# Kernel tuning notes

Hardware: AMD Instinct MI355X
Metric: run time of the kernel (lower is better)

## Reference

```python
import jax, jax.numpy as jnp
import numpy as np

B, N, S, K = 8, 4096, 1024, 16
C_IN, C_OUT = 128, 256
BN_EPS = 1e-5


def setup_inputs() -> dict:
    key = jax.random.key(0)
    ks = jax.random.split(key, 20)
    sc = 0.02
    p = {
        'xyz': jax.random.normal(ks[0], (B, N, 3), jnp.float32),
        'points': jax.random.normal(ks[1], (B, N, C_IN), jnp.float32),
        'wq': jax.random.normal(ks[2], (C_IN, C_OUT), jnp.float32) * sc,
        'wk': jax.random.normal(ks[3], (C_IN, C_OUT), jnp.float32) * sc,
        'wv': jax.random.normal(ks[4], (C_IN, C_OUT), jnp.float32) * sc,
        'dw1': jax.random.normal(ks[5], (3, C_OUT), jnp.float32) * sc,
        'db1': jnp.zeros((C_OUT,), jnp.float32),
        'dw2': jax.random.normal(ks[6], (C_OUT, C_OUT), jnp.float32) * sc,
        'db2': jnp.zeros((C_OUT,), jnp.float32),
        'gw1': jax.random.normal(ks[7], (C_OUT, C_OUT), jnp.float32) * sc,
        'gb1': jnp.zeros((C_OUT,), jnp.float32),
        'gw2': jax.random.normal(ks[8], (C_OUT, C_OUT), jnp.float32) * sc,
        'gb2': jnp.zeros((C_OUT,), jnp.float32),
        'lw': jax.random.normal(ks[9], (C_OUT, C_OUT), jnp.float32) * sc,
        'lb': jnp.zeros((C_OUT,), jnp.float32),
        'bn_g': jnp.ones((C_OUT,), jnp.float32),
        'bn_b': jnp.zeros((C_OUT,), jnp.float32),
    }
    return p


def _fps(xyz, npoint):
    # xyz: [N,3] -> farthest point sample indices [npoint] (deterministic start at 0,
    # matching torch impl with fixed seed semantics)
    n = xyz.shape[0]
    def step(carry, _):
        dist, far = carry
        centroid = xyz[far]                      # [3]
        d = jnp.sum((xyz - centroid) ** 2, -1)   # [N]
        dist = jnp.minimum(dist, d)
        return (dist, jnp.argmax(dist).astype(jnp.int32)), far
    init = (jnp.full((n,), 1e10, xyz.dtype), jnp.int32(0))
    _, idx = jax.lax.scan(step, init, None, length=npoint)
    return idx  # [npoint]


def _mlp2(x, w1, b1, w2, b2):
    return jax.nn.relu(x @ w1 + b1) @ w2 + b2


def reference(xyz, points, wq, wk, wv, dw1, db1, dw2, db2,
              gw1, gb1, gw2, gb2, lw, lb, bn_g, bn_b):
    # --- sample_and_group (FPS + KNN, knn=True) ---
    fps_idx = jax.vmap(lambda x: _fps(x, S))(xyz)                 # [B,S]
    new_xyz = jnp.take_along_axis(xyz, fps_idx[..., None], 1)     # [B,S,3]
    # squared distances sampled->all: [B,S,N]
    d2 = (jnp.sum(new_xyz**2, -1)[:, :, None]
          - 2.0 * jnp.einsum('bsc,bnc->bsn', new_xyz, xyz)
          + jnp.sum(xyz**2, -1)[:, None, :])
    knn_idx = jax.lax.top_k(-d2, K)[1]                            # [B,S,K]
    gather = jax.vmap(lambda a, i: a[i])
    knn_xyz = gather(xyz, knn_idx)                                # [B,S,K,3]
    knn_xyz_norm = knn_xyz - new_xyz[:, :, None]                  # centered coords
    knn_points = gather(points, knn_idx)                          # [B,S,K,C_in]
    sampled_points = jnp.take_along_axis(points, fps_idx[..., None], 1)  # [B,S,C_in]

    # --- vector attention ---
    q = sampled_points @ wq                                       # [B,S,C_out]
    k = knn_points @ wk                                           # [B,S,K,C_out]
    v = knn_points @ wv                                           # [B,S,K,C_out]
    pos_enc = _mlp2(knn_xyz_norm, dw1, db1, dw2, db2)             # [B,S,K,C_out]
    att = _mlp2(q[:, :, None] - k + pos_enc, gw1, gb1, gw2, gb2)  # [B,S,K,C_out]
    att = jax.nn.softmax(att / np.sqrt(C_OUT).astype(np.float32), axis=-2)
    res = jnp.einsum('bmnf,bmnf->bmf', att, v + pos_enc)          # [B,S,C_out]

    # --- fc_last + BatchNorm1d (training-mode batch stats, biased var) + ReLU ---
    res = res @ lw + lb
    mean = jnp.mean(res, axis=(0, 1))
    var = jnp.var(res, axis=(0, 1))
    res = bn_g * (res - mean) * jax.lax.rsqrt(var + BN_EPS) + bn_b
    res = jax.nn.relu(res)
    return new_xyz, res
```

## Files before the change

kernel.cpp:

```cpp
#include <hip/hip_runtime.h>

typedef unsigned long long ull;
typedef __attribute__((ext_vector_type(8))) short bf16x8;
typedef __attribute__((ext_vector_type(4))) float f32x4;

__device__ __forceinline__ unsigned short bf16b(float x){
    unsigned u = __float_as_uint(x);
    unsigned r = (u + 0x7FFFu + ((u >> 16) & 1u)) >> 16;
    return (unsigned short)r;
}
__device__ __forceinline__ float b2f(unsigned short u){
    return __uint_as_float(((unsigned)u) << 16);
}
__device__ __forceinline__ void st4(unsigned short* p, f32x4 v){
    ull pk = (ull)bf16b(v[0]) | (((ull)bf16b(v[1])) << 16)
           | (((ull)bf16b(v[2])) << 32) | (((ull)bf16b(v[3])) << 48);
    *(ull*)p = pk;
}
__device__ __forceinline__ f32x4 ld4(const unsigned short* p){
    ull pk = *(const ull*)p;
    f32x4 v;
    v[0] = b2f((unsigned short)pk);
    v[1] = b2f((unsigned short)(pk >> 16));
    v[2] = b2f((unsigned short)(pk >> 32));
    v[3] = b2f((unsigned short)(pk >> 48));
    return v;
}

#define DPPMAX(k, ctrl) do { \
    unsigned _lo = (unsigned)(k), _hi = (unsigned)((k) >> 32); \
    unsigned _l2 = (unsigned)__builtin_amdgcn_update_dpp((int)_lo, (int)_lo, (ctrl), 0xF, 0xF, false); \
    unsigned _h2 = (unsigned)__builtin_amdgcn_update_dpp((int)_hi, (int)_hi, (ctrl), 0xF, 0xF, false); \
    ull _k2 = (((ull)_h2) << 32) | _l2; \
    if (_k2 > (k)) (k) = _k2; \
} while (0)
#define DPPMIN(k, ctrl) do { \
    unsigned _lo = (unsigned)(k), _hi = (unsigned)((k) >> 32); \
    unsigned _l2 = (unsigned)__builtin_amdgcn_update_dpp((int)_lo, (int)_lo, (ctrl), 0xF, 0xF, false); \
    unsigned _h2 = (unsigned)__builtin_amdgcn_update_dpp((int)_hi, (int)_hi, (ctrl), 0xF, 0xF, false); \
    ull _k2 = (((ull)_h2) << 32) | _l2; \
    if (_k2 < (k)) (k) = _k2; \
} while (0)

template<int KT>
__device__ __forceinline__ int swz(int r, int c){
    return r * (KT * 32) + ((((c >> 3) + r) & (KT * 4 - 1)) << 3) + (c & 7);
}

template<int KT>
__device__ __forceinline__ void gemmT(const unsigned short* __restrict__ Wt,
                                      const unsigned short* __restrict__ Blds,
                                      int ch0, int lane, f32x4 acc[4][4])
{
    int i = lane & 15, q = lane >> 4;
#pragma unroll
    for (int kt = 0; kt < KT; kt++){
        int k0 = kt * 32 + q * 8;
        bf16x8 bfr[4], afr[4];
#pragma unroll
        for (int nt = 0; nt < 4; nt++)
            bfr[nt] = *(const bf16x8*)(Blds + swz<KT>(nt * 16 + i, k0));
#pragma unroll
        for (int mt = 0; mt < 4; mt++)
            afr[mt] = *(const bf16x8*)(Wt + (size_t)(ch0 + mt * 16 + i) * (KT * 32) + k0);
#pragma unroll
        for (int mt = 0; mt < 4; mt++)
#pragma unroll
            for (int nt = 0; nt < 4; nt++)
                acc[mt][nt] = __builtin_amdgcn_mfma_f32_16x16x32_bf16(afr[mt], bfr[nt], acc[mt][nt], 0, 0, 0);
    }
}

#define ZERO44(A) do { _Pragma("unroll") for (int _m = 0; _m < 4; _m++) \
    { _Pragma("unroll") for (int _n = 0; _n < 4; _n++) { A[_m][_n][0]=0.f;A[_m][_n][1]=0.f;A[_m][_n][2]=0.f;A[_m][_n][3]=0.f; } } } while(0)

#define CTRL_B(b)  ((b) << 4)
#define CTRL_AUX   (8 << 4)

__device__ __forceinline__ int ctrl_ld(const int* ctrl, int idx){
    return __hip_atomic_load(ctrl + idx, __ATOMIC_RELAXED, __HIP_MEMORY_SCOPE_AGENT);
}

__device__ __forceinline__ void knn_one(int t2, int G,
        const float* __restrict__ xyz, const float* __restrict__ nxyz,
        int* __restrict__ knn_idx, float* d2s, ull* kslot)
{
    int b = G >> 10;
    int lane = t2 & 63, wvi = t2 >> 6;
    float qx = nxyz[(size_t)G * 3], qy = nxyz[(size_t)G * 3 + 1], qz = nxyz[(size_t)G * 3 + 2];
    float qq = qx * qx + qy * qy + qz * qz;
    for (int j = 0; j < 16; j++){
        int p = t2 + (j << 8);
        const float* s = xyz + ((size_t)b * 4096 + p) * 3;
        float x = s[0], y = s[1], z = s[2];
        d2s[p] = qq - 2.f * (qx * x + qy * y + qz * z) + (x * x + y * y + z * z);
    }
    __syncthreads();
    for (int r = 0; r < 16; r++){
        ull best = ~0ull;
#pragma unroll
        for (int j = 0; j < 16; j++){
            int p = t2 + (j << 8);
            unsigned bb = __float_as_uint(d2s[p]);
            bb = (bb & 0x80000000u) ? ~bb : (bb | 0x80000000u);
            ull key = (((ull)bb) << 32) | (unsigned)p;
            if (key < best) best = key;
        }
        DPPMIN(best, 0xB1); DPPMIN(best, 0x4E); DPPMIN(best, 0x141);
        DPPMIN(best, 0x140); DPPMIN(best, 0x142); DPPMIN(best, 0x143);
        if (lane == 63) kslot[wvi] = best;
        __syncthreads();
        if (t2 == 0){
            ull bk = kslot[0];
            for (int w = 1; w < 4; w++) if (kslot[w] < bk) bk = kslot[w];
            int p = (int)(unsigned)bk;
            knn_idx[(size_t)G * 16 + r] = p;
            d2s[p] = 3.0e38f;
        }
        __syncthreads();
    }
}

__device__ void attn_unit(int t, char* base, int G0,
    const unsigned short* __restrict__ pts16,
    const float* __restrict__ xyz, const float* __restrict__ nxyz,
    const int* __restrict__ knn_idx, const float* __restrict__ qbuf,
    const unsigned short* __restrict__ wkT, const unsigned short* __restrict__ wvT,
    const unsigned short* __restrict__ dw2T, const unsigned short* __restrict__ gw1T,
    const unsigned short* __restrict__ gw2T,
    const float* __restrict__ dw1, const float* __restrict__ db1,
    const float* __restrict__ db2, const float* __restrict__ gb1, const float* __restrict__ gb2,
    unsigned short* __restrict__ resY)
{
    unsigned short* bufA = (unsigned short*)base;
    unsigned short* bufU = (unsigned short*)(base + 32768);
    int lane = t & 63, wave = t >> 6;
    int i = lane & 15, q = lane >> 4;
    int ch0 = wave * 64;
    unsigned short* ptsA = bufU;
    float* dw1s  = (float*)(bufU + 8192);
    float* db1s  = (float*)(bufU + 9728);
    float* xyznS = (float*)(bufU + 10240);
    int*   idxs  = (int*)  (bufU + 10624);

    if (t < 64) idxs[t] = knn_idx[G0 * 16 + t];
    dw1s[t] = dw1[t]; dw1s[256 + t] = dw1[256 + t]; dw1s[512 + t] = dw1[512 + t];
    db1s[t] = db1[t];
    __syncthreads();

    if (t < 64){
        int G = G0 + (t >> 4); int bb = G >> 10; int p = idxs[t];
        const float* xp = xyz + ((size_t)bb * 4096 + p) * 3;
        const float* nz = nxyz + (size_t)G * 3;
        xyznS[t * 3 + 0] = xp[0] - nz[0];
        xyznS[t * 3 + 1] = xp[1] - nz[1];
        xyznS[t * 3 + 2] = xp[2] - nz[2];
    }
    {
        int r = t >> 2, seg = t & 3;
        int G = G0 + (r >> 4); int bb = G >> 10; int p = idxs[r];
        const uint4* src = (const uint4*)(pts16 + ((size_t)bb * 4096 + p) * 128 + seg * 32);
#pragma unroll
        for (int j = 0; j < 4; j++){
            uint4 v = src[j];
            *(uint4*)(ptsA + swz<4>(r, seg * 32 + j * 8)) = v;
        }
    }
    __syncthreads();

    {
        int r = lane;
        int o0 = wave * 64;
        float x = xyznS[r * 3], y = xyznS[r * 3 + 1], z = xyznS[r * 3 + 2];
#pragma unroll
        for (int j = 0; j < 64; j += 4){
            int o = o0 + j;
            f32x4 v;
#pragma unroll
            for (int e = 0; e < 4; e++)
                v[e] = fmaxf(db1s[o + e] + x * dw1s[o + e] + y * dw1s[256 + o + e] + z * dw1s[512 + o + e], 0.f);
            st4(bufA + swz<8>(r, o), v);
        }
    }
    __syncthreads();

    f32x4 accP[4][4]; ZERO44(accP);
    gemmT<8>(dw2T, bufA, ch0, lane, accP);
#pragma unroll
    for (int mt = 0; mt < 4; mt++){
        f32x4 d2v = *(const f32x4*)(db2 + ch0 + mt * 16 + q * 4);
#pragma unroll
        for (int nt = 0; nt < 4; nt++) accP[mt][nt] += d2v;
    }
    f32x4 accK[4][4]; ZERO44(accK);
    gemmT<4>(wkT, ptsA, ch0, lane, accK);
    __syncthreads();

#pragma unroll
    for (int mt = 0; mt < 4; mt++){
        int c = ch0 + mt * 16 + q * 4;
#pragma unroll
        for (int nt = 0; nt < 4; nt++){
            int r = nt * 16 + i;
            f32x4 qv = *(const f32x4*)(qbuf + (size_t)(G0 + nt) * 256 + c);
            f32x4 tv = qv - accK[mt][nt] + accP[mt][nt];
            st4(bufA + swz<8>(r, c), tv);
        }
    }
    f32x4 accV[4][4]; ZERO44(accV);
    gemmT<4>(wvT, ptsA, ch0, lane, accV);
    __syncthreads();

#pragma unroll
    for (int mt = 0; mt < 4; mt++){
        int c = ch0 + mt * 16 + q * 4;
#pragma unroll
        for (int nt = 0; nt < 4; nt++){
            int r = nt * 16 + i;
            f32x4 uv = accV[mt][nt] + accP[mt][nt];
            st4(bufU + swz<8>(r, c), uv);
        }
    }
    f32x4 acc1[4][4]; ZERO44(acc1);
    gemmT<8>(gw1T, bufA, ch0, lane, acc1);
    __syncthreads();

#pragma unroll
    for (int mt = 0; mt < 4; mt++){
        int c = ch0 + mt * 16 + q * 4;
        f32x4 g1v = *(const f32x4*)(gb1 + c);
#pragma unroll
        for (int nt = 0; nt < 4; nt++){
            int r = nt * 16 + i;
            f32x4 av = acc1[mt][nt] + g1v;
#pragma unroll
            for (int e = 0; e < 4; e++) av[e] = fmaxf(av[e], 0.f);
            st4(bufA + swz<8>(r, c), av);
        }
    }
    __syncthreads();

    f32x4 acc2[4][4]; ZERO44(acc2);
    gemmT<8>(gw2T, bufA, ch0, lane, acc2);
    __syncthreads();

#pragma unroll
    for (int mt = 0; mt < 4; mt++){
        int c = ch0 + mt * 16 + q * 4;
        f32x4 g2v = *(const f32x4*)(gb2 + c);
#pragma unroll
        for (int nt = 0; nt < 4; nt++){
            int r = nt * 16 + i;
            f32x4 ev;
#pragma unroll
            for (int e = 0; e < 4; e++) ev[e] = __expf((acc2[mt][nt][e] + g2v[e]) * 0.0625f);
            st4(bufA + swz<8>(r, c), ev);
        }
    }
    __syncthreads();

    {
        int g = t >> 6, c4 = (t & 63) * 4;
        f32x4 num; num[0]=0.f;num[1]=0.f;num[2]=0.f;num[3]=0.f;
        f32x4 den = num;
#pragma unroll
        for (int rr = 0; rr < 16; rr++){
            int r = g * 16 + rr;
            f32x4 e4 = ld4(bufA + swz<8>(r, c4));
            f32x4 u4 = ld4(bufU + swz<8>(r, c4));
            num += e4 * u4;
            den += e4;
        }
        f32x4 rv = num / den;
        st4(resY + (size_t)(G0 + g) * 256 + c4, rv);
    }
}

__device__ void do_chunk(int t, int c, char* SM,
    const float* __restrict__ xyz, const float* __restrict__ nxyz,
    const float* __restrict__ points, const float* __restrict__ wqT,
    const int* __restrict__ fps_idx, int* __restrict__ knn_idx, float* __restrict__ qbuf,
    const unsigned short* __restrict__ pts16,
    const unsigned short* __restrict__ wkT, const unsigned short* __restrict__ wvT,
    const unsigned short* __restrict__ dw2T, const unsigned short* __restrict__ gw1T,
    const unsigned short* __restrict__ gw2T,
    const float* __restrict__ dw1, const float* __restrict__ db1,
    const float* __restrict__ db2, const float* __restrict__ gb1, const float* __restrict__ gb2,
    unsigned short* __restrict__ resY)
{
    int g0 = c * 8;
    int sub = t >> 8, t2 = t & 255;
    float* d2s = (float*)(SM + sub * 16384);
    ull* kslot = (ull*)(SM + 131072) + sub * 4;
    for (int r4 = 0; r4 < 4; r4++)
        knn_one(t2, g0 + r4 * 2 + sub, xyz, nxyz, knn_idx, d2s, kslot);
    __syncthreads();
    {
        float* sp = (float*)SM;
        if (t < 256){
            int r = t >> 5, c4 = (t & 31) * 4;
            int G = g0 + r; int b = G >> 10; int p = fps_idx[G];
            *(f32x4*)(sp + r * 128 + c4) = *(const f32x4*)(points + ((size_t)b * 4096 + p) * 128 + c4);
        }
        __syncthreads();
        float acc[4] = {0.f, 0.f, 0.f, 0.f};
        const float* wr = wqT + t2 * 128;
        for (int k = 0; k < 128; k += 4){
            f32x4 w = *(const f32x4*)(wr + k);
#pragma unroll
            for (int r = 0; r < 4; r++){
                const float* row = sp + (sub * 4 + r) * 128;
                acc[r] += w[0]*row[k] + w[1]*row[k+1] + w[2]*row[k+2] + w[3]*row[k+3];
            }
        }
#pragma unroll
        for (int r = 0; r < 4; r++) qbuf[(size_t)(g0 + sub * 4 + r) * 256 + t2] = acc[r];
        __syncthreads();
    }
    attn_unit(t2, SM + sub * 65536, g0 + sub * 4, pts16, xyz, nxyz, knn_idx, qbuf,
              wkT, wvT, dw2T, gw1T, gw2T, dw1, db1, db2, gb1, gb2, resY);
    __syncthreads();
}

__global__ void init_ctrl(int* __restrict__ ctrl)
{
    ctrl[threadIdx.x] = 0;
}

__global__ __launch_bounds__(512, 2) void mega(
    const float* __restrict__ xyz, float* __restrict__ nxyz_out, int* __restrict__ fps_idx,
    const float* __restrict__ pts, unsigned short* __restrict__ pts16,
    const float* __restrict__ wq, const float* __restrict__ wk, const float* __restrict__ wv,
    const float* __restrict__ dw2, const float* __restrict__ gw1, const float* __restrict__ gw2,
    const float* __restrict__ lw,
    float* __restrict__ wqT, unsigned short* __restrict__ wkT, unsigned short* __restrict__ wvT,
    unsigned short* __restrict__ dw2T, unsigned short* __restrict__ gw1T,
    unsigned short* __restrict__ gw2T, unsigned short* __restrict__ lwT,
    float* __restrict__ stats,
    const float* __restrict__ dw1, const float* __restrict__ db1, const float* __restrict__ db2,
    const float* __restrict__ gb1, const float* __restrict__ gb2,
    int* __restrict__ knn_idx, float* __restrict__ qbuf, unsigned short* __restrict__ resY,
    int* __restrict__ ctrl)
{
    __shared__ __align__(16) char SM[132096];
    int blk = blockIdx.x, t = threadIdx.x;

    if (blk < 8){
        int b = blk;
        int lane = t & 63, wvi = t >> 6;
        float* sx = (float*)SM;
        float* sy = (float*)(SM + 16384);
        float* sz = (float*)(SM + 32768);
        int* farS = (int*)(SM + 49152);
        ull (*slotK)[8] = (ull(*)[8])(SM + 53248);
        for (int p = t; p < 4096; p += 512){
            const float* s = xyz + ((size_t)b * 4096 + p) * 3;
            sx[p] = s[0]; sy[p] = s[1]; sz[p] = s[2];
        }
        __syncthreads();
        float px[8], py[8], pz[8], dist[8];
        unsigned nplo[8];
#pragma unroll
        for (int j = 0; j < 8; j++){
            int p = t + (j << 9);
            px[j] = sx[p]; py[j] = sy[p]; pz[j] = sz[p];
            dist[j] = 1e10f;
            nplo[j] = ~(unsigned)p;
            asm volatile("" : "+v"(px[j]), "+v"(py[j]), "+v"(pz[j]), "+v"(nplo[j]));
        }
        int far = 0;
        float cx = sx[0], cy = sy[0], cz = sz[0];
        int par = 0;
        for (int s = 0; s < 1024; s++){
            if (t == 0) farS[s] = far;
            ull lb = 0;
#pragma unroll
            for (int j = 0; j < 8; j++){
                float dx = __fsub_rn(px[j], cx);
                float dy = __fsub_rn(py[j], cy);
                float dz = __fsub_rn(pz[j], cz);
                float d = __fadd_rn(__fadd_rn(__fmul_rn(dx, dx), __fmul_rn(dy, dy)), __fmul_rn(dz, dz));
                float nd = fminf(dist[j], d);
                dist[j] = nd;
                ull k2 = (((ull)__float_as_uint(nd)) << 32) | nplo[j];
                if (k2 > lb) lb = k2;
            }
            DPPMAX(lb, 0xB1); DPPMAX(lb, 0x4E); DPPMAX(lb, 0x141);
            DPPMAX(lb, 0x140); DPPMAX(lb, 0x142); DPPMAX(lb, 0x143);
            if (lane == 63) slotK[par][wvi] = lb;
            __syncthreads();
            ull k = slotK[par][lane & 7];
            DPPMAX(k, 0xB1); DPPMAX(k, 0x4E); DPPMAX(k, 0x141);
            far = (int)(~(unsigned)k);
            cx = sx[far]; cy = sy[far]; cz = sz[far];
            if (((s & 15) == 15) && wvi == 7){
                int s0 = s - 15;
                if (lane < 16){
                    fps_idx[b * 1024 + s0 + lane] = farS[s0 + lane];
                } else {
                    int idx = lane - 16;
                    int st = s0 + idx / 3, d = idx - (idx / 3) * 3;
                    int f = farS[st];
                    float v = (d == 0) ? sx[f] : ((d == 1) ? sy[f] : sz[f]);
                    nxyz_out[(size_t)b * 3072 + st * 3 + d] = v;
                }
                if (lane == 0)
                    __hip_atomic_store(ctrl + CTRL_B(b), s + 1,
                                       __ATOMIC_RELEASE, __HIP_MEMORY_SCOPE_AGENT);
            }
            par ^= 1;
        }
        if (t == 0){ while (ctrl_ld(ctrl, CTRL_AUX) < 248) __builtin_amdgcn_s_sleep(16); }
        __syncthreads();
        __threadfence();
        do_chunk(t, b * 128 + 127, SM, xyz, nxyz_out, pts, wqT, fps_idx, knn_idx, qbuf,
                 pts16, wkT, wvT, dw2T, gw1T, gw2T, dw1, db1, db2, gb1, gb2, resY);
        return;
    }

    int w = blk - 8;
    for (int base = w; base < 704; base += 248){
        if (base == 0) stats[t & 511] = 0.f;
        int i = base * 512 + t;
        if (i < 32768){ int n = i >> 7, kk = i & 127; wqT[i] = wq[kk * 256 + n]; }
        else if (i < 65536){ int j = i - 32768; int n = j >> 7, kk = j & 127; wkT[j] = bf16b(wk[kk * 256 + n]); }
        else if (i < 98304){ int j = i - 65536; int n = j >> 7, kk = j & 127; wvT[j] = bf16b(wv[kk * 256 + n]); }
        else if (i < 163840){ int j = i - 98304; int n = j >> 8, kk = j & 255; dw2T[j] = bf16b(dw2[kk * 256 + n]); }
        else if (i < 229376){ int j = i - 163840; int n = j >> 8, kk = j & 255; gw1T[j] = bf16b(gw1[kk * 256 + n]); }
        else if (i < 294912){ int j = i - 229376; int n = j >> 8, kk = j & 255; gw2T[j] = bf16b(gw2[kk * 256 + n]); }
        else { int j = i - 294912; int n = j >> 8, kk = j & 255; lwT[j] = bf16b(lw[kk * 256 + n]); }
    }
    for (int base = w; base < 2048; base += 248){
        int i = (base * 512 + t) * 4;
        f32x4 v = *(const f32x4*)(pts + i);
        ull pk = (ull)bf16b(v[0]) | (((ull)bf16b(v[1])) << 16)
               | (((ull)bf16b(v[2])) << 32) | (((ull)bf16b(v[3])) << 48);
        *(ull*)(pts16 + i) = pk;
    }
    __threadfence();
    __syncthreads();
    if (t == 0){
        atomicAdd(ctrl + CTRL_AUX, 1);
        while (ctrl_ld(ctrl, CTRL_AUX) < 248) __builtin_amdgcn_s_sleep(16);
    }
    __syncthreads();
    __threadfence();
    for (int j = 0; j < 5; j++){
        int p = w + 248 * j;
        if (p >= 1016) break;
        int bb = p & 7, cc = p >> 3;
        int need = cc * 8 + 8;
        if (t == 0){ while (ctrl_ld(ctrl, CTRL_B(bb)) < need) __builtin_amdgcn_s_sleep(8); }
        __syncthreads();
        __threadfence();
        do_chunk(t, bb * 128 + cc, SM, xyz, nxyz_out, pts, wqT, fps_idx, knn_idx, qbuf,
                 pts16, wkT, wvT, dw2T, gw1T, gw2T, dw1, db1, db2, gb1, gb2, resY);
    }
}

__global__ __launch_bounds__(256, 2) void z_gemm(const unsigned short* __restrict__ resY,
                                                 const unsigned short* __restrict__ lwT,
                                                 const float* __restrict__ lb,
                                                 float* __restrict__ zbuf,
                                                 float* __restrict__ stats)
{
    int t = threadIdx.x, lane = t & 63, wave = t >> 6;
    int i = lane & 15, q = lane >> 4;
    int row0 = blockIdx.x * 128;
    int ch0 = wave * 64;
    f32x4 acc[4][8];
#pragma unroll
    for (int mt = 0; mt < 4; mt++)
#pragma unroll
        for (int nt = 0; nt < 8; nt++){ acc[mt][nt][0]=0.f;acc[mt][nt][1]=0.f;acc[mt][nt][2]=0.f;acc[mt][nt][3]=0.f; }
#pragma unroll
    for (int kt = 0; kt < 8; kt++){
        int k0 = kt * 32 + q * 8;
        bf16x8 a[4], bb[8];
#pragma unroll
        for (int mt = 0; mt < 4; mt++)
            a[mt] = *(const bf16x8*)(lwT + (size_t)(ch0 + mt * 16 + i) * 256 + k0);
#pragma unroll
        for (int nt = 0; nt < 8; nt++)
            bb[nt] = *(const bf16x8*)(resY + (size_t)(row0 + nt * 16 + i) * 256 + k0);
#pragma unroll
        for (int mt = 0; mt < 4; mt++)
#pragma unroll
            for (int nt = 0; nt < 8; nt++)
                acc[mt][nt] = __builtin_amdgcn_mfma_f32_16x16x32_bf16(a[mt], bb[nt], acc[mt][nt], 0, 0, 0);
    }
    f32x4 s1[4], s2[4];
#pragma unroll
    for (int mt = 0; mt < 4; mt++){ s1[mt][0]=0.f;s1[mt][1]=0.f;s1[mt][2]=0.f;s1[mt][3]=0.f; s2[mt]=s1[mt]; }
#pragma unroll
    for (int mt = 0; mt < 4; mt++){
        int c = ch0 + mt * 16 + q * 4;
        f32x4 lb4 = *(const f32x4*)(lb + c);
#pragma unroll
        for (int nt = 0; nt < 8; nt++){
            int r = row0 + nt * 16 + i;
            f32x4 z = acc[mt][nt] + lb4;
            *(f32x4*)(zbuf + (size_t)r * 256 + c) = z;
            s1[mt] += z;
            s2[mt] += z * z;
        }
    }
    for (int m = 1; m < 16; m <<= 1){
#pragma unroll
        for (int mt = 0; mt < 4; mt++)
#pragma unroll
            for (int e = 0; e < 4; e++){
                s1[mt][e] += __shfl_xor(s1[mt][e], m);
                s2[mt][e] += __shfl_xor(s2[mt][e], m);
            }
    }
    if (i == 0){
#pragma unroll
        for (int mt = 0; mt < 4; mt++){
            int c = ch0 + mt * 16 + q * 4;
#pragma unroll
            for (int e = 0; e < 4; e++){
                atomicAdd(&stats[c + e], s1[mt][e]);
                atomicAdd(&stats[256 + c + e], s2[mt][e]);
            }
        }
    }
}

__global__ __launch_bounds__(256) void bn_kernel(const float* __restrict__ zbuf,
                                                 const float* __restrict__ stats,
                                                 const float* __restrict__ bn_g,
                                                 const float* __restrict__ bn_b,
                                                 float* __restrict__ out)
{
    int G = blockIdx.x, c = threadIdx.x;
    float mean = stats[c] * (1.f / 8192.f);
    float var = stats[256 + c] * (1.f / 8192.f) - mean * mean;
    float inv = rsqrtf(var + 1e-5f);
    float z = zbuf[(size_t)G * 256 + c];
    float y = bn_g[c] * (z - mean) * inv + bn_b[c];
    out[24576 + (size_t)G * 256 + c] = fmaxf(y, 0.f);
}

extern "C" void kernel_launch(void* const* d_in, const int* in_sizes, int n_in,
                              void* d_out, int out_size, void* d_ws, size_t ws_size,
                              hipStream_t stream)
{
    const float* xyz    = (const float*)d_in[0];
    const float* points = (const float*)d_in[1];
    const float* wq  = (const float*)d_in[2];
    const float* wk  = (const float*)d_in[3];
    const float* wv  = (const float*)d_in[4];
    const float* dw1 = (const float*)d_in[5];
    const float* db1 = (const float*)d_in[6];
    const float* dw2 = (const float*)d_in[7];
    const float* db2 = (const float*)d_in[8];
    const float* gw1 = (const float*)d_in[9];
    const float* gb1 = (const float*)d_in[10];
    const float* gw2 = (const float*)d_in[11];
    const float* gb2 = (const float*)d_in[12];
    const float* lw  = (const float*)d_in[13];
    const float* lb  = (const float*)d_in[14];
    const float* bn_g = (const float*)d_in[15];
    const float* bn_b = (const float*)d_in[16];
    float* out = (float*)d_out;

    char* ws = (char*)d_ws;
    int*            fps_idx = (int*)(ws + 0);
    int*            knn_idx = (int*)(ws + 32768);
    float*          qbuf    = (float*)(ws + 557056);
    unsigned short* pts16   = (unsigned short*)(ws + 8945664);
    unsigned short* wkT     = (unsigned short*)(ws + 17334272);
    unsigned short* wvT     = (unsigned short*)(ws + 17399808);
    unsigned short* dw2T    = (unsigned short*)(ws + 17465344);
    unsigned short* gw1T    = (unsigned short*)(ws + 17596416);
    unsigned short* gw2T    = (unsigned short*)(ws + 17727488);
    unsigned short* lwT     = (unsigned short*)(ws + 17858560);
    float*          wqT     = (float*)(ws + 17989632);
    unsigned short* resY    = (unsigned short*)(ws + 18120704);
    float*          zbuf    = (float*)(ws + 22315008);
    float*          stats   = (float*)(ws + 30703616);
    int*            ctrl    = (int*)(ws + 22315008);

    init_ctrl<<<1, 256, 0, stream>>>(ctrl);
    mega<<<256, 512, 0, stream>>>(xyz, out, fps_idx, points, pts16,
                                  wq, wk, wv, dw2, gw1, gw2, lw,
                                  wqT, wkT, wvT, dw2T, gw1T, gw2T, lwT, stats,
                                  dw1, db1, db2, gb1, gb2,
                                  knn_idx, qbuf, resY, ctrl);
    z_gemm<<<64, 256, 0, stream>>>(resY, lwT, lb, zbuf, stats);
    bn_kernel<<<8192, 256, 0, stream>>>(zbuf, stats, bn_g, bn_b, out);
}
```

Before: 989.9 us.

## Replace per-batch FPS progress counter with sentinel-polled data readiness

Consumer blocks used to wait on a per-batch release counter before each chunk. Now fps_idx and new_xyz are pre-filled with -1 sentinels, the FPS producer writes them with relaxed atomic stores, and each consumer polls the exact 8 indices and 24 coordinates it needs, caching them in LDS. This drops the release-store/acquire handshake and the per-chunk global reads of nxyz. In exchange it relies on relaxed ordering of individual words and adds a wider init kernel.

```diff
diff --git a/kernel.cpp b/kernel.cpp
--- a/kernel.cpp
+++ b/kernel.cpp
@@ -74,20 +74,21 @@
 #define ZERO44(A) do { _Pragma("unroll") for (int _m = 0; _m < 4; _m++) \
     { _Pragma("unroll") for (int _n = 0; _n < 4; _n++) { A[_m][_n][0]=0.f;A[_m][_n][1]=0.f;A[_m][_n][2]=0.f;A[_m][_n][3]=0.f; } } } while(0)
 
-#define CTRL_B(b)  ((b) << 4)
 #define CTRL_AUX   (8 << 4)
 
-__device__ __forceinline__ int ctrl_ld(const int* ctrl, int idx){
-    return __hip_atomic_load(ctrl + idx, __ATOMIC_RELAXED, __HIP_MEMORY_SCOPE_AGENT);
-}
-
-__device__ __forceinline__ void knn_one(int t2, int G,
-        const float* __restrict__ xyz, const float* __restrict__ nxyz,
+__device__ __forceinline__ int ald(const int* p){
+    return __hip_atomic_load(p, __ATOMIC_RELAXED, __HIP_MEMORY_SCOPE_AGENT);
+}
+__device__ __forceinline__ void ast(int* p, int v){
+    __hip_atomic_store(p, v, __ATOMIC_RELAXED, __HIP_MEMORY_SCOPE_AGENT);
+}
+
+__device__ __forceinline__ void knn_one(int t2, int G, float qx, float qy, float qz,
+        const float* __restrict__ xyz,
         int* __restrict__ knn_idx, float* d2s, ull* kslot)
 {
     int b = G >> 10;
     int lane = t2 & 63, wvi = t2 >> 6;
-    float qx = nxyz[(size_t)G * 3], qy = nxyz[(size_t)G * 3 + 1], qz = nxyz[(size_t)G * 3 + 2];
     float qq = qx * qx + qy * qy + qz * qz;
     for (int j = 0; j < 16; j++){
         int p = t2 + (j << 8);
@@ -121,9 +122,9 @@
     }
 }
 
-__device__ void attn_unit(int t, char* base, int G0,
+__device__ void attn_unit(int t, char* base, int G0, const float* nxL4,
     const unsigned short* __restrict__ pts16,
-    const float* __restrict__ xyz, const float* __restrict__ nxyz,
+    const float* __restrict__ xyz,
     const int* __restrict__ knn_idx, const float* __restrict__ qbuf,
     const unsigned short* __restrict__ wkT, const unsigned short* __restrict__ wvT,
     const unsigned short* __restrict__ dw2T, const unsigned short* __restrict__ gw1T,
@@ -151,7 +152,7 @@
     if (t < 64){
         int G = G0 + (t >> 4); int bb = G >> 10; int p = idxs[t];
         const float* xp = xyz + ((size_t)bb * 4096 + p) * 3;
-        const float* nz = nxyz + (size_t)G * 3;
+        const float* nz = nxL4 + (t >> 4) * 3;
         xyznS[t * 3 + 0] = xp[0] - nz[0];
         xyznS[t * 3 + 1] = xp[1] - nz[1];
         xyznS[t * 3 + 2] = xp[2] - nz[2];
@@ -290,16 +291,38 @@
 {
     int g0 = c * 8;
     int sub = t >> 8, t2 = t & 255;
+    int*   fpsL = (int*)  (SM + 131200);
+    float* nxL  = (float*)(SM + 131232);
+    if (t < 64){
+        for (;;){
+            int v = 0; bool ok = true;
+            if (t < 8){
+                v = ald(fps_idx + g0 + t); ok = (v != -1);
+            } else if (t < 32){
+                v = ald((const int*)nxyz + (size_t)g0 * 3 + (t - 8)); ok = (v != (int)0xFFFFFFFF);
+            }
+            if (__ballot(ok) == ~0ull){
+                if (t < 8) fpsL[t] = v;
+                else if (t < 32) ((int*)nxL)[t - 8] = v;
+                break;
+            }
+            __builtin_amdgcn_s_sleep(8);
+        }
+    }
+    __syncthreads();
     float* d2s = (float*)(SM + sub * 16384);
     ull* kslot = (ull*)(SM + 131072) + sub * 4;
-    for (int r4 = 0; r4 < 4; r4++)
-        knn_one(t2, g0 + r4 * 2 + sub, xyz, nxyz, knn_idx, d2s, kslot);
+    for (int r4 = 0; r4 < 4; r4++){
+        int gl = r4 * 2 + sub;
+        knn_one(t2, g0 + gl, nxL[gl * 3], nxL[gl * 3 + 1], nxL[gl * 3 + 2],
+                xyz, knn_idx, d2s, kslot);
+    }
     __syncthreads();
     {
         float* sp = (float*)SM;
         if (t < 256){
             int r = t >> 5, c4 = (t & 31) * 4;
-            int G = g0 + r; int b = G >> 10; int p = fps_idx[G];
+            int G = g0 + r; int b = G >> 10; int p = fpsL[r];
             *(f32x4*)(sp + r * 128 + c4) = *(const f32x4*)(points + ((size_t)b * 4096 + p) * 128 + c4);
         }
         __syncthreads();
@@ -317,14 +340,19 @@
         for (int r = 0; r < 4; r++) qbuf[(size_t)(g0 + sub * 4 + r) * 256 + t2] = acc[r];
         __syncthreads();
     }
-    attn_unit(t2, SM + sub * 65536, g0 + sub * 4, pts16, xyz, nxyz, knn_idx, qbuf,
+    attn_unit(t2, SM + sub * 65536, g0 + sub * 4, nxL + sub * 12, pts16, xyz, knn_idx, qbuf,
               wkT, wvT, dw2T, gw1T, gw2T, dw1, db1, db2, gb1, gb2, resY);
     __syncthreads();
 }
 
-__global__ void init_ctrl(int* __restrict__ ctrl)
-{
-    ctrl[threadIdx.x] = 0;
+__global__ __launch_bounds__(256) void init_ws(int* __restrict__ ctrl,
+                                               int* __restrict__ fps_idx,
+                                               int* __restrict__ nxyz_i)
+{
+    int i = blockIdx.x * 256 + threadIdx.x;
+    if (i < 256) ctrl[i] = 0;
+    if (i < 8192) fps_idx[i] = -1;
+    if (i < 24576) nxyz_i[i] = (int)0xFFFFFFFF;
 }
 
 __global__ __launch_bounds__(512, 2) void mega(
@@ -396,21 +424,18 @@
             if (((s & 15) == 15) && wvi == 7){
                 int s0 = s - 15;
                 if (lane < 16){
-                    fps_idx[b * 1024 + s0 + lane] = farS[s0 + lane];
+                    ast(fps_idx + b * 1024 + s0 + lane, farS[s0 + lane]);
                 } else {
                     int idx = lane - 16;
                     int st = s0 + idx / 3, d = idx - (idx / 3) * 3;
                     int f = farS[st];
                     float v = (d == 0) ? sx[f] : ((d == 1) ? sy[f] : sz[f]);
-                    nxyz_out[(size_t)b * 3072 + st * 3 + d] = v;
+                    ast((int*)nxyz_out + (size_t)b * 3072 + st * 3 + d, __float_as_int(v));
                 }
-                if (lane == 0)
-                    __hip_atomic_store(ctrl + CTRL_B(b), s + 1,
-                                       __ATOMIC_RELEASE, __HIP_MEMORY_SCOPE_AGENT);
             }
             par ^= 1;
         }
-        if (t == 0){ while (ctrl_ld(ctrl, CTRL_AUX) < 248) __builtin_amdgcn_s_sleep(16); }
+        if (t == 0){ while (ald(ctrl + CTRL_AUX) < 248) __builtin_amdgcn_s_sleep(16); }
         __syncthreads();
         __threadfence();
         do_chunk(t, b * 128 + 127, SM, xyz, nxyz_out, pts, wqT, fps_idx, knn_idx, qbuf,
@@ -441,7 +466,7 @@
     __syncthreads();
     if (t == 0){
         atomicAdd(ctrl + CTRL_AUX, 1);
-        while (ctrl_ld(ctrl, CTRL_AUX) < 248) __builtin_amdgcn_s_sleep(16);
+        while (ald(ctrl + CTRL_AUX) < 248) __builtin_amdgcn_s_sleep(16);
     }
     __syncthreads();
     __threadfence();
@@ -449,10 +474,6 @@
         int p = w + 248 * j;
         if (p >= 1016) break;
         int bb = p & 7, cc = p >> 3;
-        int need = cc * 8 + 8;
-        if (t == 0){ while (ctrl_ld(ctrl, CTRL_B(bb)) < need) __builtin_amdgcn_s_sleep(8); }
-        __syncthreads();
-        __threadfence();
         do_chunk(t, bb * 128 + cc, SM, xyz, nxyz_out, pts, wqT, fps_idx, knn_idx, qbuf,
                  pts16, wkT, wvT, dw2T, gw1T, gw2T, dw1, db1, db2, gb1, gb2, resY);
     }
@@ -582,7 +603,7 @@
     float*          stats   = (float*)(ws + 30703616);
     int*            ctrl    = (int*)(ws + 22315008);
 
-    init_ctrl<<<1, 256, 0, stream>>>(ctrl);
+    init_ws<<<96, 256, 0, stream>>>(ctrl, fps_idx, (int*)out);
     mega<<<256, 512, 0, stream>>>(xyz, out, fps_idx, points, pts16,
                                   wq, wk, wv, dw2, gw1, gw2, lw,
                                   wqT, wkT, wvT, dw2T, gw1T, gw2T, lwT, stats,
```

Result: faster. 926.4 us (-6.4%).
